# Kernel optimization log

Hardware: AMD Instinct MI355X
Metric: run time of the kernel (lower is better)

The kernel has to match this reference:

```python
import jax, jax.numpy as jnp
import numpy as np

H = 50  # hidden size

def _lstm_last_h(x, W_ih, W_hh, b_ih, b_hh):
    """Run a single-layer LSTM (PyTorch gate order i,f,g,o) over x [B,T,1],
    return final hidden state h_T [B,H]. Zero initial (h, c)."""
    B = x.shape[0]
    h0 = jnp.zeros((B, H), dtype=x.dtype)
    c0 = jnp.zeros((B, H), dtype=x.dtype)
    b = b_ih + b_hh  # [4H]

    def step(carry, xt):
        h, c = carry
        # gates: [B,4H]
        gates = xt @ W_ih.T + h @ W_hh.T + b
        i, f, g, o = jnp.split(gates, 4, axis=-1)
        i = jax.nn.sigmoid(i)
        f = jax.nn.sigmoid(f)
        g = jnp.tanh(g)
        o = jax.nn.sigmoid(o)
        c = f * c + i * g
        h = o * jnp.tanh(c)
        return (h, c), None

    xt = jnp.swapaxes(x, 0, 1)  # [T,B,1]
    (hT, _), _ = jax.lax.scan(step, (h0, c0), xt)
    return hT


def setup_inputs() -> dict:
    key = jax.random.key(0)
    ks = jax.random.split(key, 7)
    B, T = 1024, 96
    s = 1.0 / np.sqrt(H)  # PyTorch LSTM init scale
    return {
        "x": jax.random.normal(ks[0], (B, T, 1), dtype=jnp.float32),
        "W_ih": jax.random.uniform(ks[1], (4 * H, 1), jnp.float32, -s, s),
        "W_hh": jax.random.uniform(ks[2], (4 * H, H), jnp.float32, -s, s),
        "b_ih": jax.random.uniform(ks[3], (4 * H,), jnp.float32, -s, s),
        "b_hh": jax.random.uniform(ks[4], (4 * H,), jnp.float32, -s, s),
        "W_fc": jax.random.uniform(ks[5], (1, H), jnp.float32, -s, s),
        "b_fc": jax.random.uniform(ks[6], (1,), jnp.float32, -s, s),
        "num_pred": 12,
    }


def reference(x, W_ih, W_hh, b_ih, b_hh, W_fc, b_fc, num_pred):
    preds = []
    for _ in range(num_pred):  # static loop over prediction horizon
        hT = _lstm_last_h(x, W_ih, W_hh, b_ih, b_hh)        # [B,H]
        out = hT @ W_fc.T + b_fc                            # [B,1]
        preds.append(out[:, 0])
        # append prediction as next input, drop oldest timestep (window slides)
        x = jnp.concatenate([x, out[:, :, None]], axis=1)[:, 1:, :]
    return jnp.stack(preds, axis=1)  # [B, num_pred]
```

## Files before the change

### kernel.cpp

```cpp
#include <hip/hip_runtime.h>
#include <stdint.h>


#define HSZ 50
#define TLEN 96

#define GRP(WT,A0,A1,A2,A3,IL,IH,FL,FH,GL,GH,OL,OH,BL,BH,POST) \
    "s_waitcnt lgkmcnt(" WT ")\n\t" \
    "v_pk_fma_f32 v[" A0 "], v[" IL "], v[" BL "], v[" A0 "]\n\t" \
    "v_pk_fma_f32 v[" A1 "], v[" FL "], v[" BL "], v[" A1 "]\n\t" \
    "v_pk_fma_f32 v[" A2 "], v[" GL "], v[" BL "], v[" A2 "]\n\t" \
    "v_pk_fma_f32 v[" A3 "], v[" OL "], v[" BL "], v[" A3 "]\n\t" \
    "v_pk_fma_f32 v[" A0 "], v[" IH "], v[" BH "], v[" A0 "]\n\t" \
    "v_pk_fma_f32 v[" A1 "], v[" FH "], v[" BH "], v[" A1 "]\n\t" \
    "v_pk_fma_f32 v[" A2 "], v[" GH "], v[" BH "], v[" A2 "]\n\t" \
    "v_pk_fma_f32 v[" A3 "], v[" OH "], v[" BH "], v[" A3 "]\n\t" \
    POST

#define GRPM(WT,A0,A1,A2,A3,IL,IH,FL,FH,GL,GH,OL,OH,BL,BH,POST) \
    "s_waitcnt lgkmcnt(" WT ")\n\t" \
    "v_pk_mul_f32 v[" A0 "], v[" IL "], v[" BL "]\n\t" \
    "v_pk_mul_f32 v[" A1 "], v[" FL "], v[" BL "]\n\t" \
    "v_pk_mul_f32 v[" A2 "], v[" GL "], v[" BL "]\n\t" \
    "v_pk_mul_f32 v[" A3 "], v[" OL "], v[" BL "]\n\t" \
    "v_pk_fma_f32 v[" A0 "], v[" IH "], v[" BH "], v[" A0 "]\n\t" \
    "v_pk_fma_f32 v[" A1 "], v[" FH "], v[" BH "], v[" A1 "]\n\t" \
    "v_pk_fma_f32 v[" A2 "], v[" GH "], v[" BH "], v[" A2 "]\n\t" \
    "v_pk_fma_f32 v[" A3 "], v[" OH "], v[" BH "], v[" A3 "]\n\t" \
    POST

#define GRPX(...)  GRP(__VA_ARGS__)
#define GRPMX(...) GRPM(__VA_ARGS__)
#define SOLOX(...) SOLO(__VA_ARGS__)

#define PA "22:23","24:25","26:27","28:29"
#define PB "30:31","32:33","34:35","36:37"
#define PC "38:39","40:41","42:43","44:45"
#define W0  "48:49","50:51","100:101","102:103","152:153","154:155","204:205","206:207"
#define W1  "52:53","54:55","104:105","106:107","156:157","158:159","208:209","210:211"
#define W2  "56:57","58:59","108:109","110:111","160:161","162:163","212:213","214:215"
#define W3  "60:61","62:63","112:113","114:115","164:165","166:167","216:217","218:219"
#define W4  "64:65","66:67","116:117","118:119","168:169","170:171","220:221","222:223"
#define W5  "68:69","70:71","120:121","122:123","172:173","174:175","224:225","226:227"
#define W6  "72:73","74:75","124:125","126:127","176:177","178:179","228:229","230:231"
#define W7  "76:77","78:79","128:129","130:131","180:181","182:183","232:233","234:235"
#define W8  "80:81","82:83","132:133","134:135","184:185","186:187","236:237","238:239"
#define W9  "84:85","86:87","136:137","138:139","188:189","190:191","240:241","242:243"
#define W10 "88:89","90:91","140:141","142:143","192:193","194:195","244:245","246:247"
#define W11 "92:93","94:95","144:145","146:147","196:197","198:199","248:249","250:251"
#define W12 "96:97","98:99","148:149","150:151","200:201","202:203","252:253","254:255"
#define B0 "0:1","2:3"
#define B1 "4:5","6:7"
#define B2 "8:9","10:11"
#define B3 "12:13","14:15"

#define SOLO(XOFF,XW,CR,HNW,H0,H1,H2,H3,H4,H5,H6,H7,H8,H9,H10,H11,H12) \
    "ds_read_b32 v12, v19 offset:" XOFF "\n\t" \
    "s_waitcnt lgkmcnt(0)\n\t" \
    "ds_write_b32 v20, v12 offset:" XW "\n\t" \
    "ds_read_b128 v[0:3], v20 offset:" H0 "\n\t" \
    "ds_read_b128 v[4:7], v20 offset:" H1 "\n\t" \
    GRPMX("1", PA, W0, B0, "ds_read_b128 v[0:3], v20 offset:" H2 "\n\t") \
    GRPX("1", PA, W1,  B1, "ds_read_b128 v[4:7], v20 offset:" H3 "\n\t") \
    GRPX("1", PA, W2,  B0, "ds_read_b128 v[0:3], v20 offset:" H4 "\n\t") \
    GRPX("1", PA, W3,  B1, "ds_read_b128 v[4:7], v20 offset:" H5 "\n\t") \
    GRPX("1", PA, W4,  B0, "ds_read_b128 v[0:3], v20 offset:" H6 "\n\t") \
    GRPX("1", PA, W5,  B1, "ds_read_b128 v[4:7], v20 offset:" H7 "\n\t") \
    GRPX("1", PA, W6,  B0, "ds_read_b128 v[0:3], v20 offset:" H8 "\n\t") \
    GRPX("1", PA, W7,  B1, "ds_read_b128 v[4:7], v20 offset:" H9 "\n\t") \
    GRPX("1", PA, W8,  B0, "ds_read_b128 v[0:3], v20 offset:" H10 "\n\t") \
    GRPX("1", PA, W9,  B1, "ds_read_b128 v[4:7], v20 offset:" H11 "\n\t") \
    GRPX("1", PA, W10, B0, "ds_read_b128 v[0:3], v20 offset:" H12 "\n\t") \
    GRPX("1", PA, W11, B1, "") \
    GRPX("0", PA, W12, B0, "") \
    "v_add_f32 v22, v22, v23\n\t" \
    "v_add_f32 v24, v24, v25\n\t" \
    "v_add_f32 v26, v26, v27\n\t" \
    "v_add_f32 v28, v28, v29\n\t" \
    "v_mul_f32 v23, 0xbfb8aa3b, v22\n\t" \
    "v_mul_f32 v25, 0xbfb8aa3b, v24\n\t" \
    "v_mul_f32 v27, 0x4038aa3b, v26\n\t" \
    "v_mul_f32 v29, 0xbfb8aa3b, v28\n\t" \
    "v_exp_f32 v23, v23\n\t" "v_exp_f32 v25, v25\n\t" \
    "v_exp_f32 v27, v27\n\t" "v_exp_f32 v29, v29\n\t" \
    "v_add_f32 v23, 1.0, v23\n\t" "v_add_f32 v25, 1.0, v25\n\t" \
    "v_add_f32 v27, 1.0, v27\n\t" "v_add_f32 v29, 1.0, v29\n\t" \
    "v_rcp_f32 v23, v23\n\t" "v_rcp_f32 v25, v25\n\t" \
    "v_rcp_f32 v27, v27\n\t" "v_rcp_f32 v29, v29\n\t" \
    "s_nop 1\n\t" \
    "v_fma_f32 v27, -2.0, v27, 1.0\n\t" \
    "v_mul_f32 v22, v23, v27\n\t" \
    "v_fma_f32 " CR ", v25, " CR ", v22\n\t" \
    "v_mul_f32 v24, 0x4038aa3b, " CR "\n\t" \
    "v_exp_f32 v24, v24\n\t" \
    "s_nop 1\n\t" \
    "v_add_f32 v24, 1.0, v24\n\t" \
    "v_rcp_f32 v24, v24\n\t" \
    "s_nop 1\n\t" \
    "v_fma_f32 v24, -2.0, v24, 1.0\n\t" \
    "v_mul_f32 v22, v29, v24\n\t" \
    "ds_write_b32 v21, v22 offset:" HNW "\n\t"

#define HA "0","16","32","48","64","80","96","112","128","144","160","176","192"
#define HB "256","272","288","304","320","336","352","368","384","400","416","432","448"
#define HC "512","528","544","560","576","592","608","624","640","656","672","688","704"

#define FC(PREDOFF) \
    "v_mul_f32 v26, v22, v46\n\t" \
    "s_nop 1\n\t" \
    "ds_swizzle_b32 v27, v26 offset:0x041F\n\t" \
    "s_waitcnt lgkmcnt(0)\n\t" \
    "v_add_f32 v26, v26, v27\n\t" \
    "ds_swizzle_b32 v27, v26 offset:0x081F\n\t" \
    "s_waitcnt lgkmcnt(0)\n\t" \
    "v_add_f32 v26, v26, v27\n\t" \
    "ds_swizzle_b32 v27, v26 offset:0x101F\n\t" \
    "s_waitcnt lgkmcnt(0)\n\t" \
    "v_add_f32 v26, v26, v27\n\t" \
    "ds_swizzle_b32 v27, v26 offset:0x201F\n\t" \
    "s_waitcnt lgkmcnt(0)\n\t" \
    "v_add_f32 v26, v26, v27\n\t" \
    "ds_swizzle_b32 v27, v26 offset:0x401F\n\t" \
    "s_waitcnt lgkmcnt(0)\n\t" \
    "v_add_f32 v26, v26, v27\n\t" \
    "s_nop 1\n\t" \
    "v_readlane_b32 s26, v26, 0\n\t" \
    "v_readlane_b32 s27, v26, 32\n\t" \
    "s_nop 4\n\t" \
    "v_mov_b32 v27, s26\n\t" \
    "v_add_f32 v27, s27, v27\n\t" \
    "v_add_f32 v27, s25, v27\n\t" \
    "ds_write_b32 v19, v27 offset:" PREDOFF "\n\t"

__global__ __attribute__((amdgpu_flat_work_group_size(64, 64),
                          amdgpu_waves_per_eu(1, 1)))
void rec_lstm_kernel(const float* __restrict__ x,
                     const float* __restrict__ W_ih,
                     const float* __restrict__ W_hh,
                     const float* __restrict__ b_ih,
                     const float* __restrict__ b_hh,
                     const float* __restrict__ W_fc,
                     const float* __restrict__ b_fc,
                     const int*   __restrict__ num_pred,
                     float*       __restrict__ out)
{
    const int b = blockIdx.x;
    const int j = threadIdx.x;

    __shared__ __align__(16) float lds[304];
    if (j < 48) { lds[192 + j] = x[b*TLEN + j]; lds[192 + j + 48] = x[b*TLEN + j + 48]; }

    const int NP = num_pred[0];
    const int nt = NP / 3;
    const uint32_t lb = (uint32_t)(uintptr_t)&lds[0];

    asm volatile(
        "s_load_dword s25, %[bfcp], 0x0\n\t"
        "s_waitcnt lgkmcnt(0)\n\t"
        "v_mbcnt_lo_u32_b32 v0, -1, 0\n\t"
        "v_mbcnt_hi_u32_b32 v0, -1, v0\n\t"
        "s_mov_b32 s22, 49\n\t"
        "v_min_u32 v1, s22, v0\n\t"
        "s_mov_b32 s22, 200\n\t"
        "v_mul_lo_u32 v2, s22, v1\n\t"
        "s_mov_b32 s22, 10000\n\t"
        "v_add_u32 v3, s22, v2\n\t"
        "s_mov_b32 s22, 20000\n\t"
        "v_add_u32 v4, s22, v2\n\t"
        "s_mov_b32 s22, 30000\n\t"
        "v_add_u32 v5, s22, v2\n\t"
        "v_lshlrev_b32 v6, 2, v1\n\t"
        "global_load_dword v48,  v6, %[bih]\n\t"
        "global_load_dword v100, v6, %[bih] offset:200\n\t"
        "global_load_dword v152, v6, %[bih] offset:400\n\t"
        "global_load_dword v204, v6, %[bih] offset:600\n\t"
        "global_load_dword v7,  v6, %[bhh]\n\t"
        "global_load_dword v8,  v6, %[bhh] offset:200\n\t"
        "global_load_dword v9,  v6, %[bhh] offset:400\n\t"
        "global_load_dword v10, v6, %[bhh] offset:600\n\t"
        "global_load_dword v49,  v6, %[wih]\n\t"
        "global_load_dword v101, v6, %[wih] offset:200\n\t"
        "global_load_dword v153, v6, %[wih] offset:400\n\t"
        "global_load_dword v205, v6, %[wih] offset:600\n\t"
        "global_load_dword v46, v6, %[wfcp]\n\t"
        "global_load_dwordx4 v[50:53], v2, %[whh]\n\t"
        "global_load_dwordx4 v[54:57], v2, %[whh] offset:16\n\t"
        "global_load_dwordx4 v[58:61], v2, %[whh] offset:32\n\t"
        "global_load_dwordx4 v[62:65], v2, %[whh] offset:48\n\t"
        "global_load_dwordx4 v[66:69], v2, %[whh] offset:64\n\t"
        "global_load_dwordx4 v[70:73], v2, %[whh] offset:80\n\t"
        "global_load_dwordx4 v[74:77], v2, %[whh] offset:96\n\t"
        "global_load_dwordx4 v[78:81], v2, %[whh] offset:112\n\t"
        "global_load_dwordx4 v[82:85], v2, %[whh] offset:128\n\t"
        "global_load_dwordx4 v[86:89], v2, %[whh] offset:144\n\t"
        "global_load_dwordx4 v[90:93], v2, %[whh] offset:160\n\t"
        "global_load_dwordx4 v[94:97], v2, %[whh] offset:176\n\t"
        "global_load_dwordx2 v[98:99], v2, %[whh] offset:192\n\t"
        "global_load_dwordx4 v[102:105], v3, %[whh]\n\t"
        "global_load_dwordx4 v[106:109], v3, %[whh] offset:16\n\t"
        "global_load_dwordx4 v[110:113], v3, %[whh] offset:32\n\t"
        "global_load_dwordx4 v[114:117], v3, %[whh] offset:48\n\t"
        "global_load_dwordx4 v[118:121], v3, %[whh] offset:64\n\t"
        "global_load_dwordx4 v[122:125], v3, %[whh] offset:80\n\t"
        "global_load_dwordx4 v[126:129], v3, %[whh] offset:96\n\t"
        "global_load_dwordx4 v[130:133], v3, %[whh] offset:112\n\t"
        "global_load_dwordx4 v[134:137], v3, %[whh] offset:128\n\t"
        "global_load_dwordx4 v[138:141], v3, %[whh] offset:144\n\t"
        "global_load_dwordx4 v[142:145], v3, %[whh] offset:160\n\t"
        "global_load_dwordx4 v[146:149], v3, %[whh] offset:176\n\t"
        "global_load_dwordx2 v[150:151], v3, %[whh] offset:192\n\t"
        "global_load_dwordx4 v[154:157], v4, %[whh]\n\t"
        "global_load_dwordx4 v[158:161], v4, %[whh] offset:16\n\t"
        "global_load_dwordx4 v[162:165], v4, %[whh] offset:32\n\t"
        "global_load_dwordx4 v[166:169], v4, %[whh] offset:48\n\t"
        "global_load_dwordx4 v[170:173], v4, %[whh] offset:64\n\t"
        "global_load_dwordx4 v[174:177], v4, %[whh] offset:80\n\t"
        "global_load_dwordx4 v[178:181], v4, %[whh] offset:96\n\t"
        "global_load_dwordx4 v[182:185], v4, %[whh] offset:112\n\t"
        "global_load_dwordx4 v[186:189], v4, %[whh] offset:128\n\t"
        "global_load_dwordx4 v[190:193], v4, %[whh] offset:144\n\t"
        "global_load_dwordx4 v[194:197], v4, %[whh] offset:160\n\t"
        "global_load_dwordx4 v[198:201], v4, %[whh] offset:176\n\t"
        "global_load_dwordx2 v[202:203], v4, %[whh] offset:192\n\t"
        "global_load_dwordx4 v[206:209], v5, %[whh]\n\t"
        "global_load_dwordx4 v[210:213], v5, %[whh] offset:16\n\t"
        "global_load_dwordx4 v[214:217], v5, %[whh] offset:32\n\t"
        "global_load_dwordx4 v[218:221], v5, %[whh] offset:48\n\t"
        "global_load_dwordx4 v[222:225], v5, %[whh] offset:64\n\t"
        "global_load_dwordx4 v[226:229], v5, %[whh] offset:80\n\t"
        "global_load_dwordx4 v[230:233], v5, %[whh] offset:96\n\t"
        "global_load_dwordx4 v[234:237], v5, %[whh] offset:112\n\t"
        "global_load_dwordx4 v[238:241], v5, %[whh] offset:128\n\t"
        "global_load_dwordx4 v[242:245], v5, %[whh] offset:144\n\t"
        "global_load_dwordx4 v[246:249], v5, %[whh] offset:160\n\t"
        "global_load_dwordx4 v[250:253], v5, %[whh] offset:176\n\t"
        "global_load_dwordx2 v[254:255], v5, %[whh] offset:192\n\t"
        "s_waitcnt vmcnt(0)\n\t"
        "v_add_f32 v48,  v48,  v7\n\t"
        "v_add_f32 v100, v100, v8\n\t"
        "v_add_f32 v152, v152, v9\n\t"
        "v_add_f32 v204, v204, v10\n\t"
        "v_cmp_gt_u32 vcc, 50, v0\n\t"
        "v_cndmask_b32 v46, 0, v46, vcc\n\t"
        "v_mov_b32 v20, %[lb]\n\t"
        "v_lshl_add_u32 v21, v1, 2, v20\n\t"
        "v_add_u32 v21, 8, v21\n\t"
        "v_add_u32 v19, 0x300, v20\n\t"
        "s_mov_b32 s21, %[nt]\n\t"
        "4:\n\t"
        "v_mov_b32 v16, 0\n\t"
        "v_mov_b32 v17, 0\n\t"
        "v_mov_b32 v18, 0\n\t"
        "v_mov_b32 v5, 0\n\t"
        "v_mov_b32 v6, 1.0\n\t"
        "ds_write_b32 v21, v5\n\t"
        "ds_write_b32 v21, v5 offset:256\n\t"
        "ds_write_b32 v21, v5 offset:512\n\t"
        "ds_write_b32 v20, v6\n\t"
        "ds_write_b32 v20, v6 offset:256\n\t"
        "ds_write_b32 v20, v6 offset:512\n\t"
        "ds_read_b32 v12, v19 offset:0\n\t"
        "ds_read_b32 v13, v19 offset:4\n\t"
        "ds_read_b32 v14, v19 offset:8\n\t"
        "s_waitcnt lgkmcnt(0)\n\t"
        "ds_write_b32 v20, v12 offset:4\n\t"
        "ds_write_b32 v20, v13 offset:260\n\t"
        "ds_write_b32 v20, v14 offset:516\n\t"
        "v_add_u32 v19, 4, v19\n\t"
        "ds_read_b128 v[0:3],   v20 offset:0\n\t"
        "ds_read_b128 v[4:7],   v20 offset:256\n\t"
        "ds_read_b128 v[8:11],  v20 offset:512\n\t"
        "ds_read_b128 v[12:15], v20 offset:16\n\t"
        "s_mov_b32 s20, 94\n\t"
        "3:\n\t"
        GRPMX("3", PA, W0,  B0, "ds_read_b128 v[0:3],   v20 offset:272\n\t")
        GRPMX("3", PB, W0,  B1, "ds_read_b128 v[4:7],   v20 offset:528\n\t")
        GRPMX("3", PC, W0,  B2, "ds_read_b128 v[8:11],  v20 offset:32\n\t")
        GRPX("3", PA, W1,  B3, "ds_read_b128 v[12:15], v20 offset:288\n\t")
        GRPX("3", PB, W1,  B0, "ds_read_b128 v[0:3],   v20 offset:544\n\t")
        GRPX("3", PC, W1,  B1, "ds_read_b128 v[4:7],   v20 offset:48\n\t")
        GRPX("3", PA, W2,  B2, "ds_read_b128 v[8:11],  v20 offset:304\n\t")
        GRPX("3", PB, W2,  B3, "ds_read_b128 v[12:15], v20 offset:560\n\t")
        GRPX("3", PC, W2,  B0, "ds_read_b128 v[0:3],   v20 offset:64\n\t")
        GRPX("3", PA, W3,  B1, "ds_read_b128 v[4:7],   v20 offset:320\n\t")
        GRPX("3", PB, W3,  B2, "ds_read_b128 v[8:11],  v20 offset:576\n\t")
        GRPX("3", PC, W3,  B3, "ds_read_b128 v[12:15], v20 offset:80\n\t")
        GRPX("3", PA, W4,  B0, "ds_read_b128 v[0:3],   v20 offset:336\n\t")
        GRPX("3", PB, W4,  B1, "ds_read_b128 v[4:7],   v20 offset:592\n\t")
        GRPX("3", PC, W4,  B2, "ds_read_b128 v[8:11],  v20 offset:96\n\t")
        GRPX("3", PA, W5,  B3, "ds_read_b128 v[12:15], v20 offset:352\n\t")
        GRPX("3", PB, W5,  B0, "ds_read_b128 v[0:3],   v20 offset:608\n\t")
        GRPX("3", PC, W5,  B1, "ds_read_b128 v[4:7],   v20 offset:112\n\t")
        GRPX("3", PA, W6,  B2, "ds_read_b128 v[8:11],  v20 offset:368\n\t")
        GRPX("3", PB, W6,  B3, "ds_read_b128 v[12:15], v20 offset:624\n\t")
        GRPX("3", PC, W6,  B0, "ds_read_b128 v[0:3],   v20 offset:128\n\t")
        GRPX("3", PA, W7,  B1, "ds_read_b128 v[4:7],   v20 offset:384\n\t")
        GRPX("3", PB, W7,  B2, "ds_read_b128 v[8:11],  v20 offset:640\n\t")
        GRPX("3", PC, W7,  B3, "ds_read_b128 v[12:15], v20 offset:144\n\t")
        GRPX("3", PA, W8,  B0, "ds_read_b128 v[0:3],   v20 offset:400\n\t")
        GRPX("3", PB, W8,  B1, "ds_read_b128 v[4:7],   v20 offset:656\n\t")
        GRPX("3", PC, W8,  B2, "ds_read_b128 v[8:11],  v20 offset:160\n\t")
        GRPX("3", PA, W9,  B3, "ds_read_b128 v[12:15], v20 offset:416\n\t")
        GRPX("3", PB, W9,  B0, "ds_read_b128 v[0:3],   v20 offset:672\n\t")
        GRPX("3", PC, W9,  B1, "ds_read_b128 v[4:7],   v20 offset:176\n\t")
        GRPX("3", PA, W10, B2, "ds_read_b128 v[8:11],  v20 offset:432\n\t")
        GRPX("3", PB, W10, B3, "ds_read_b128 v[12:15], v20 offset:688\n\t")
        GRPX("3", PC, W10, B0, "ds_read_b128 v[0:3],   v20 offset:192\n\t")
        GRPX("3", PA, W11, B1, "ds_read_b128 v[4:7],   v20 offset:448\n\t")
        GRPX("3", PB, W11, B2, "ds_read_b128 v[8:11],  v20 offset:704\n\t")
        GRPX("3", PC, W11, B3, "")
        "ds_read_b32 v12, v19 offset:0\n\t"
        "ds_read_b32 v13, v19 offset:4\n\t"
        "ds_read_b32 v14, v19 offset:8\n\t"
        GRPX("5", PA, W12, B0, "")
        GRPX("4", PB, W12, B1, "")
        GRPX("3", PC, W12, B2, "")
        "v_add_f32 v22, v22, v23\n\t" "v_add_f32 v24, v24, v25\n\t"
        "v_add_f32 v26, v26, v27\n\t" "v_add_f32 v28, v28, v29\n\t"
        "v_add_f32 v30, v30, v31\n\t" "v_add_f32 v32, v32, v33\n\t"
        "v_add_f32 v34, v34, v35\n\t" "v_add_f32 v36, v36, v37\n\t"
        "v_add_f32 v38, v38, v39\n\t" "v_add_f32 v40, v40, v41\n\t"
        "v_add_f32 v42, v42, v43\n\t" "v_add_f32 v44, v44, v45\n\t"
        "v_mul_f32 v23, 0xbfb8aa3b, v22\n\t"
        "v_mul_f32 v31, 0xbfb8aa3b, v30\n\t"
        "v_mul_f32 v39, 0xbfb8aa3b, v38\n\t"
        "v_mul_f32 v25, 0xbfb8aa3b, v24\n\t"
        "v_mul_f32 v33, 0xbfb8aa3b, v32\n\t"
        "v_mul_f32 v41, 0xbfb8aa3b, v40\n\t"
        "v_mul_f32 v27, 0x4038aa3b, v26\n\t"
        "v_mul_f32 v35, 0x4038aa3b, v34\n\t"
        "v_mul_f32 v43, 0x4038aa3b, v42\n\t"
        "v_mul_f32 v29, 0xbfb8aa3b, v28\n\t"
        "v_mul_f32 v37, 0xbfb8aa3b, v36\n\t"
        "v_mul_f32 v45, 0xbfb8aa3b, v44\n\t"
        "v_exp_f32 v23, v23\n\t" "v_exp_f32 v31, v31\n\t" "v_exp_f32 v39, v39\n\t"
        "v_exp_f32 v25, v25\n\t" "v_exp_f32 v33, v33\n\t" "v_exp_f32 v41, v41\n\t"
        "v_exp_f32 v27, v27\n\t" "v_exp_f32 v35, v35\n\t" "v_exp_f32 v43, v43\n\t"
        "v_exp_f32 v29, v29\n\t" "v_exp_f32 v37, v37\n\t" "v_exp_f32 v45, v45\n\t"
        "v_add_f32 v23, 1.0, v23\n\t" "v_add_f32 v31, 1.0, v31\n\t" "v_add_f32 v39, 1.0, v39\n\t"
        "v_add_f32 v25, 1.0, v25\n\t" "v_add_f32 v33, 1.0, v33\n\t" "v_add_f32 v41, 1.0, v41\n\t"
        "v_add_f32 v27, 1.0, v27\n\t" "v_add_f32 v35, 1.0, v35\n\t" "v_add_f32 v43, 1.0, v43\n\t"
        "v_add_f32 v29, 1.0, v29\n\t" "v_add_f32 v37, 1.0, v37\n\t" "v_add_f32 v45, 1.0, v45\n\t"
        "v_rcp_f32 v23, v23\n\t" "v_rcp_f32 v31, v31\n\t" "v_rcp_f32 v39, v39\n\t"
        "v_rcp_f32 v25, v25\n\t" "v_rcp_f32 v33, v33\n\t" "v_rcp_f32 v41, v41\n\t"
        "v_rcp_f32 v27, v27\n\t" "v_rcp_f32 v35, v35\n\t" "v_rcp_f32 v43, v43\n\t"
        "v_rcp_f32 v29, v29\n\t" "v_rcp_f32 v37, v37\n\t" "v_rcp_f32 v45, v45\n\t"
        "v_fma_f32 v27, -2.0, v27, 1.0\n\t"
        "v_fma_f32 v35, -2.0, v35, 1.0\n\t"
        "v_fma_f32 v43, -2.0, v43, 1.0\n\t"
        "v_mul_f32 v22, v23, v27\n\t"
        "v_mul_f32 v30, v31, v35\n\t"
        "v_mul_f32 v38, v39, v43\n\t"
        "v_fma_f32 v16, v25, v16, v22\n\t"
        "v_fma_f32 v17, v33, v17, v30\n\t"
        "v_fma_f32 v18, v41, v18, v38\n\t"
        "v_mul_f32 v24, 0x4038aa3b, v16\n\t"
        "v_mul_f32 v32, 0x4038aa3b, v17\n\t"
        "v_mul_f32 v40, 0x4038aa3b, v18\n\t"
        "v_exp_f32 v24, v24\n\t" "v_exp_f32 v32, v32\n\t" "v_exp_f32 v40, v40\n\t"
        "v_add_f32 v24, 1.0, v24\n\t" "v_add_f32 v32, 1.0, v32\n\t" "v_add_f32 v40, 1.0, v40\n\t"
        "v_rcp_f32 v24, v24\n\t" "v_rcp_f32 v32, v32\n\t" "v_rcp_f32 v40, v40\n\t"
        "s_nop 0\n\t"
        "v_fma_f32 v24, -2.0, v24, 1.0\n\t"
        "v_fma_f32 v32, -2.0, v32, 1.0\n\t"
        "v_fma_f32 v40, -2.0, v40, 1.0\n\t"
        "v_mul_f32 v22, v29, v24\n\t"
        "v_mul_f32 v30, v37, v32\n\t"
        "v_mul_f32 v38, v45, v40\n\t"
        "ds_write_b32 v21, v22\n\t"
        "ds_write_b32 v21, v30 offset:256\n\t"
        "ds_write_b32 v21, v38 offset:512\n\t"
        "s_waitcnt lgkmcnt(3)\n\t"
        "ds_write_b32 v20, v12 offset:4\n\t"
        "ds_write_b32 v20, v13 offset:260\n\t"
        "ds_write_b32 v20, v14 offset:516\n\t"
        "v_add_u32 v19, 4, v19\n\t"
        "ds_read_b128 v[0:3],   v20 offset:0\n\t"
        "ds_read_b128 v[4:7],   v20 offset:256\n\t"
        "ds_read_b128 v[8:11],  v20 offset:512\n\t"
        "ds_read_b128 v[12:15], v20 offset:16\n\t"
        "s_sub_u32 s20, s20, 1\n\t"
        "s_cmp_lg_u32 s20, 0\n\t"
        "s_cbranch_scc1 3b\n\t"
        "s_waitcnt lgkmcnt(0)\n\t"
        "v_add_u32 v19, -8, v19\n\t"
        SOLOX("4",  "4",   "v16", "0",   HA)
        SOLOX("8",  "4",   "v16", "0",   HA)
        FC("12")
        SOLOX("8",  "260", "v17", "256", HB)
        SOLOX("12", "260", "v17", "256", HB)
        FC("16")
        SOLOX("12", "516", "v18", "512", HC)
        SOLOX("16", "516", "v18", "512", HC)
        FC("20")
        "s_waitcnt lgkmcnt(0)\n\t"
        "v_add_u32 v19, 0xfffffe98, v19\n\t"
        "s_sub_u32 s21, s21, 1\n\t"
        "s_cmp_lg_u32 s21, 0\n\t"
        "s_cbranch_scc1 4b\n\t"
        :
        : [lb] "v"(lb), [nt] "s"(nt),
          [whh] "s"(W_hh), [wih] "s"(W_ih), [bih] "s"(b_ih), [bhh] "s"(b_hh),
          [wfcp] "s"(W_fc), [bfcp] "s"(b_fc)
        : "memory", "scc", "vcc", "s20", "s21", "s22", "s25", "s26", "s27",
          "v0","v1","v2","v3","v4","v5","v6","v7","v8","v9","v10","v11",
          "v12","v13","v14","v15","v16","v17","v18","v19","v20","v21","v22",
          "v23","v24","v25","v26","v27","v28","v29","v30","v31","v32","v33",
          "v34","v35","v36","v37","v38","v39","v40","v41","v42","v43","v44",
          "v45","v46",
          "v48","v49","v50","v51","v52","v53","v54","v55","v56","v57","v58",
          "v59","v60","v61","v62","v63","v64","v65","v66","v67","v68","v69",
          "v70","v71","v72","v73","v74","v75","v76","v77","v78","v79","v80",
          "v81","v82","v83","v84","v85","v86","v87","v88","v89","v90","v91",
          "v92","v93","v94","v95","v96","v97","v98","v99","v100","v101",
          "v102","v103","v104","v105","v106","v107","v108","v109","v110",
          "v111","v112","v113","v114","v115","v116","v117","v118","v119",
          "v120","v121","v122","v123","v124","v125","v126","v127","v128",
          "v129","v130","v131","v132","v133","v134","v135","v136","v137",
          "v138","v139","v140","v141","v142","v143","v144","v145","v146",
          "v147","v148","v149","v150","v151","v152","v153","v154","v155",
          "v156","v157","v158","v159","v160","v161","v162","v163","v164",
          "v165","v166","v167","v168","v169","v170","v171","v172","v173",
          "v174","v175","v176","v177","v178","v179","v180","v181","v182",
          "v183","v184","v185","v186","v187","v188","v189","v190","v191",
          "v192","v193","v194","v195","v196","v197","v198","v199","v200",
          "v201","v202","v203","v204","v205","v206","v207","v208","v209",
          "v210","v211","v212","v213","v214","v215","v216","v217","v218",
          "v219","v220","v221","v222","v223","v224","v225","v226","v227",
          "v228","v229","v230","v231","v232","v233","v234","v235","v236",
          "v237","v238","v239","v240","v241","v242","v243","v244","v245",
          "v246","v247","v248","v249","v250","v251","v252","v253","v254",
          "v255");

    if (j < NP) out[b * NP + j] = lds[192 + TLEN + j];
}

extern "C" void kernel_launch(void* const* d_in, const int* in_sizes, int n_in,
                              void* d_out, int out_size, void* d_ws, size_t ws_size,
                              hipStream_t stream)
{
    const float* x    = (const float*)d_in[0];
    const float* W_ih = (const float*)d_in[1];
    const float* W_hh = (const float*)d_in[2];
    const float* b_ih = (const float*)d_in[3];
    const float* b_hh = (const float*)d_in[4];
    const float* W_fc = (const float*)d_in[5];
    const float* b_fc = (const float*)d_in[6];
    const int*   np   = (const int*)d_in[7];
    float* out = (float*)d_out;

    const int B = in_sizes[0] / TLEN;
    rec_lstm_kernel<<<B, 64, 0, stream>>>(x, W_ih, W_hh, b_ih, b_hh,
                                          W_fc, b_fc, np, out);
}
```

Baseline: 495.1 us.

## Replace three-chain interleaved LSTM recurrence with single chain and deeper LDS prefetch

The old kernel interleaved three independent prediction chains (PA/PB/PC) so one chain's math could hide another's latency, then ran serial SOLO steps at the tail. The new code runs one prediction at a time with a single accumulator set. It issues all seven h-vector LDS reads up front, with more in flight per step, and drops the staggered SOLO tail logic. This gives a simpler schedule and fewer LDS buffers, but removes the instruction-level parallelism that hid the latency of the exp/rcp and LDS round-trip on the serial dependence chain.

```diff
diff --git a/kernel.cpp b/kernel.cpp
--- a/kernel.cpp
+++ b/kernel.cpp
@@ -16,7 +16,6 @@
     "v_pk_fma_f32 v[" A2 "], v[" GH "], v[" BH "], v[" A2 "]\n\t" \
     "v_pk_fma_f32 v[" A3 "], v[" OH "], v[" BH "], v[" A3 "]\n\t" \
     POST
-
 #define GRPM(WT,A0,A1,A2,A3,IL,IH,FL,FH,GL,GH,OL,OH,BL,BH,POST) \
     "s_waitcnt lgkmcnt(" WT ")\n\t" \
     "v_pk_mul_f32 v[" A0 "], v[" IL "], v[" BL "]\n\t" \
@@ -28,14 +27,10 @@
     "v_pk_fma_f32 v[" A2 "], v[" GH "], v[" BH "], v[" A2 "]\n\t" \
     "v_pk_fma_f32 v[" A3 "], v[" OH "], v[" BH "], v[" A3 "]\n\t" \
     POST
-
 #define GRPX(...)  GRP(__VA_ARGS__)
 #define GRPMX(...) GRPM(__VA_ARGS__)
-#define SOLOX(...) SOLO(__VA_ARGS__)
-
-#define PA "22:23","24:25","26:27","28:29"
-#define PB "30:31","32:33","34:35","36:37"
-#define PC "38:39","40:41","42:43","44:45"
+
+#define ACC "28:29","30:31","32:33","34:35"
 #define W0  "48:49","50:51","100:101","102:103","152:153","154:155","204:205","206:207"
 #define W1  "52:53","54:55","104:105","106:107","156:157","158:159","208:209","210:211"
 #define W2  "56:57","58:59","108:109","110:111","160:161","162:163","212:213","214:215"
@@ -49,88 +44,13 @@
 #define W10 "88:89","90:91","140:141","142:143","192:193","194:195","244:245","246:247"
 #define W11 "92:93","94:95","144:145","146:147","196:197","198:199","248:249","250:251"
 #define W12 "96:97","98:99","148:149","150:151","200:201","202:203","252:253","254:255"
-#define B0 "0:1","2:3"
-#define B1 "4:5","6:7"
-#define B2 "8:9","10:11"
-#define B3 "12:13","14:15"
-
-#define SOLO(XOFF,XW,CR,HNW,H0,H1,H2,H3,H4,H5,H6,H7,H8,H9,H10,H11,H12) \
-    "ds_read_b32 v12, v19 offset:" XOFF "\n\t" \
-    "s_waitcnt lgkmcnt(0)\n\t" \
-    "ds_write_b32 v20, v12 offset:" XW "\n\t" \
-    "ds_read_b128 v[0:3], v20 offset:" H0 "\n\t" \
-    "ds_read_b128 v[4:7], v20 offset:" H1 "\n\t" \
-    GRPMX("1", PA, W0, B0, "ds_read_b128 v[0:3], v20 offset:" H2 "\n\t") \
-    GRPX("1", PA, W1,  B1, "ds_read_b128 v[4:7], v20 offset:" H3 "\n\t") \
-    GRPX("1", PA, W2,  B0, "ds_read_b128 v[0:3], v20 offset:" H4 "\n\t") \
-    GRPX("1", PA, W3,  B1, "ds_read_b128 v[4:7], v20 offset:" H5 "\n\t") \
-    GRPX("1", PA, W4,  B0, "ds_read_b128 v[0:3], v20 offset:" H6 "\n\t") \
-    GRPX("1", PA, W5,  B1, "ds_read_b128 v[4:7], v20 offset:" H7 "\n\t") \
-    GRPX("1", PA, W6,  B0, "ds_read_b128 v[0:3], v20 offset:" H8 "\n\t") \
-    GRPX("1", PA, W7,  B1, "ds_read_b128 v[4:7], v20 offset:" H9 "\n\t") \
-    GRPX("1", PA, W8,  B0, "ds_read_b128 v[0:3], v20 offset:" H10 "\n\t") \
-    GRPX("1", PA, W9,  B1, "ds_read_b128 v[4:7], v20 offset:" H11 "\n\t") \
-    GRPX("1", PA, W10, B0, "ds_read_b128 v[0:3], v20 offset:" H12 "\n\t") \
-    GRPX("1", PA, W11, B1, "") \
-    GRPX("0", PA, W12, B0, "") \
-    "v_add_f32 v22, v22, v23\n\t" \
-    "v_add_f32 v24, v24, v25\n\t" \
-    "v_add_f32 v26, v26, v27\n\t" \
-    "v_add_f32 v28, v28, v29\n\t" \
-    "v_mul_f32 v23, 0xbfb8aa3b, v22\n\t" \
-    "v_mul_f32 v25, 0xbfb8aa3b, v24\n\t" \
-    "v_mul_f32 v27, 0x4038aa3b, v26\n\t" \
-    "v_mul_f32 v29, 0xbfb8aa3b, v28\n\t" \
-    "v_exp_f32 v23, v23\n\t" "v_exp_f32 v25, v25\n\t" \
-    "v_exp_f32 v27, v27\n\t" "v_exp_f32 v29, v29\n\t" \
-    "v_add_f32 v23, 1.0, v23\n\t" "v_add_f32 v25, 1.0, v25\n\t" \
-    "v_add_f32 v27, 1.0, v27\n\t" "v_add_f32 v29, 1.0, v29\n\t" \
-    "v_rcp_f32 v23, v23\n\t" "v_rcp_f32 v25, v25\n\t" \
-    "v_rcp_f32 v27, v27\n\t" "v_rcp_f32 v29, v29\n\t" \
-    "s_nop 1\n\t" \
-    "v_fma_f32 v27, -2.0, v27, 1.0\n\t" \
-    "v_mul_f32 v22, v23, v27\n\t" \
-    "v_fma_f32 " CR ", v25, " CR ", v22\n\t" \
-    "v_mul_f32 v24, 0x4038aa3b, " CR "\n\t" \
-    "v_exp_f32 v24, v24\n\t" \
-    "s_nop 1\n\t" \
-    "v_add_f32 v24, 1.0, v24\n\t" \
-    "v_rcp_f32 v24, v24\n\t" \
-    "s_nop 1\n\t" \
-    "v_fma_f32 v24, -2.0, v24, 1.0\n\t" \
-    "v_mul_f32 v22, v29, v24\n\t" \
-    "ds_write_b32 v21, v22 offset:" HNW "\n\t"
-
-#define HA "0","16","32","48","64","80","96","112","128","144","160","176","192"
-#define HB "256","272","288","304","320","336","352","368","384","400","416","432","448"
-#define HC "512","528","544","560","576","592","608","624","640","656","672","688","704"
-
-#define FC(PREDOFF) \
-    "v_mul_f32 v26, v22, v46\n\t" \
-    "s_nop 1\n\t" \
-    "ds_swizzle_b32 v27, v26 offset:0x041F\n\t" \
-    "s_waitcnt lgkmcnt(0)\n\t" \
-    "v_add_f32 v26, v26, v27\n\t" \
-    "ds_swizzle_b32 v27, v26 offset:0x081F\n\t" \
-    "s_waitcnt lgkmcnt(0)\n\t" \
-    "v_add_f32 v26, v26, v27\n\t" \
-    "ds_swizzle_b32 v27, v26 offset:0x101F\n\t" \
-    "s_waitcnt lgkmcnt(0)\n\t" \
-    "v_add_f32 v26, v26, v27\n\t" \
-    "ds_swizzle_b32 v27, v26 offset:0x201F\n\t" \
-    "s_waitcnt lgkmcnt(0)\n\t" \
-    "v_add_f32 v26, v26, v27\n\t" \
-    "ds_swizzle_b32 v27, v26 offset:0x401F\n\t" \
-    "s_waitcnt lgkmcnt(0)\n\t" \
-    "v_add_f32 v26, v26, v27\n\t" \
-    "s_nop 1\n\t" \
-    "v_readlane_b32 s26, v26, 0\n\t" \
-    "v_readlane_b32 s27, v26, 32\n\t" \
-    "s_nop 4\n\t" \
-    "v_mov_b32 v27, s26\n\t" \
-    "v_add_f32 v27, s27, v27\n\t" \
-    "v_add_f32 v27, s25, v27\n\t" \
-    "ds_write_b32 v19, v27 offset:" PREDOFF "\n\t"
+#define SL0 "0:1","2:3"
+#define SL1 "4:5","6:7"
+#define SL2 "8:9","10:11"
+#define SL3 "12:13","14:15"
+#define SL4 "16:17","18:19"
+#define SL5 "20:21","22:23"
+#define SL6 "24:25","26:27"
 
 __global__ __attribute__((amdgpu_flat_work_group_size(64, 64),
                           amdgpu_waves_per_eu(1, 1)))
@@ -147,11 +67,10 @@
     const int b = blockIdx.x;
     const int j = threadIdx.x;
 
-    __shared__ __align__(16) float lds[304];
-    if (j < 48) { lds[192 + j] = x[b*TLEN + j]; lds[192 + j + 48] = x[b*TLEN + j + 48]; }
+    __shared__ __align__(16) float lds[176];
+    if (j < 48) { lds[64 + j] = x[b*TLEN + j]; lds[64 + j + 48] = x[b*TLEN + j + 48]; }
 
     const int NP = num_pred[0];
-    const int nt = NP / 3;
     const uint32_t lb = (uint32_t)(uintptr_t)&lds[0];
 
     asm volatile(
@@ -182,7 +101,7 @@
         "global_load_dword v101, v6, %[wih] offset:200\n\t"
         "global_load_dword v153, v6, %[wih] offset:400\n\t"
         "global_load_dword v205, v6, %[wih] offset:600\n\t"
-        "global_load_dword v46, v6, %[wfcp]\n\t"
+        "global_load_dword v41, v6, %[wfcp]\n\t"
         "global_load_dwordx4 v[50:53], v2, %[whh]\n\t"
         "global_load_dwordx4 v[54:57], v2, %[whh] offset:16\n\t"
         "global_load_dwordx4 v[58:61], v2, %[whh] offset:32\n\t"
@@ -241,165 +160,121 @@
         "v_add_f32 v152, v152, v9\n\t"
         "v_add_f32 v204, v204, v10\n\t"
         "v_cmp_gt_u32 vcc, 50, v0\n\t"
-        "v_cndmask_b32 v46, 0, v46, vcc\n\t"
-        "v_mov_b32 v20, %[lb]\n\t"
-        "v_lshl_add_u32 v21, v1, 2, v20\n\t"
-        "v_add_u32 v21, 8, v21\n\t"
-        "v_add_u32 v19, 0x300, v20\n\t"
-        "s_mov_b32 s21, %[nt]\n\t"
+        "v_cndmask_b32 v41, 0, v41, vcc\n\t"
+        "v_mov_b32 v38, %[lb]\n\t"
+        "v_lshl_add_u32 v39, v1, 2, v38\n\t"
+        "v_add_u32 v39, 8, v39\n\t"
+        "v_add_u32 v40, 0x100, v38\n\t"
+        "v_mov_b32 v44, 1.0\n\t"
+        "ds_write_b32 v38, v44\n\t"
+        "s_mov_b32 s21, %[np]\n\t"
         "4:\n\t"
-        "v_mov_b32 v16, 0\n\t"
-        "v_mov_b32 v17, 0\n\t"
-        "v_mov_b32 v18, 0\n\t"
-        "v_mov_b32 v5, 0\n\t"
-        "v_mov_b32 v6, 1.0\n\t"
-        "ds_write_b32 v21, v5\n\t"
-        "ds_write_b32 v21, v5 offset:256\n\t"
-        "ds_write_b32 v21, v5 offset:512\n\t"
-        "ds_write_b32 v20, v6\n\t"
-        "ds_write_b32 v20, v6 offset:256\n\t"
-        "ds_write_b32 v20, v6 offset:512\n\t"
-        "ds_read_b32 v12, v19 offset:0\n\t"
-        "ds_read_b32 v13, v19 offset:4\n\t"
-        "ds_read_b32 v14, v19 offset:8\n\t"
-        "s_waitcnt lgkmcnt(0)\n\t"
-        "ds_write_b32 v20, v12 offset:4\n\t"
-        "ds_write_b32 v20, v13 offset:260\n\t"
-        "ds_write_b32 v20, v14 offset:516\n\t"
-        "v_add_u32 v19, 4, v19\n\t"
-        "ds_read_b128 v[0:3],   v20 offset:0\n\t"
-        "ds_read_b128 v[4:7],   v20 offset:256\n\t"
-        "ds_read_b128 v[8:11],  v20 offset:512\n\t"
-        "ds_read_b128 v[12:15], v20 offset:16\n\t"
-        "s_mov_b32 s20, 94\n\t"
+        "v_mov_b32 v36, 0\n\t"
+        "v_mov_b32 v44, 0\n\t"
+        "ds_write_b32 v39, v44\n\t"
+        "ds_read_b32 v42, v40\n\t"
+        "s_waitcnt lgkmcnt(0)\n\t"
+        "ds_write_b32 v38, v42 offset:4\n\t"
+        "ds_read_b128 v[0:3],   v38 offset:0\n\t"
+        "ds_read_b128 v[4:7],   v38 offset:16\n\t"
+        "ds_read_b128 v[8:11],  v38 offset:32\n\t"
+        "ds_read_b128 v[12:15], v38 offset:48\n\t"
+        "ds_read_b128 v[16:19], v38 offset:64\n\t"
+        "ds_read_b128 v[20:23], v38 offset:80\n\t"
+        "ds_read_b128 v[24:27], v38 offset:96\n\t"
+        "s_mov_b32 s20, 96\n\t"
         "3:\n\t"
-        GRPMX("3", PA, W0,  B0, "ds_read_b128 v[0:3],   v20 offset:272\n\t")
-        GRPMX("3", PB, W0,  B1, "ds_read_b128 v[4:7],   v20 offset:528\n\t")
-        GRPMX("3", PC, W0,  B2, "ds_read_b128 v[8:11],  v20 offset:32\n\t")
-        GRPX("3", PA, W1,  B3, "ds_read_b128 v[12:15], v20 offset:288\n\t")
-        GRPX("3", PB, W1,  B0, "ds_read_b128 v[0:3],   v20 offset:544\n\t")
-        GRPX("3", PC, W1,  B1, "ds_read_b128 v[4:7],   v20 offset:48\n\t")
-        GRPX("3", PA, W2,  B2, "ds_read_b128 v[8:11],  v20 offset:304\n\t")
-        GRPX("3", PB, W2,  B3, "ds_read_b128 v[12:15], v20 offset:560\n\t")
-        GRPX("3", PC, W2,  B0, "ds_read_b128 v[0:3],   v20 offset:64\n\t")
-        GRPX("3", PA, W3,  B1, "ds_read_b128 v[4:7],   v20 offset:320\n\t")
-        GRPX("3", PB, W3,  B2, "ds_read_b128 v[8:11],  v20 offset:576\n\t")
-        GRPX("3", PC, W3,  B3, "ds_read_b128 v[12:15], v20 offset:80\n\t")
-        GRPX("3", PA, W4,  B0, "ds_read_b128 v[0:3],   v20 offset:336\n\t")
-        GRPX("3", PB, W4,  B1, "ds_read_b128 v[4:7],   v20 offset:592\n\t")
-        GRPX("3", PC, W4,  B2, "ds_read_b128 v[8:11],  v20 offset:96\n\t")
-        GRPX("3", PA, W5,  B3, "ds_read_b128 v[12:15], v20 offset:352\n\t")
-        GRPX("3", PB, W5,  B0, "ds_read_b128 v[0:3],   v20 offset:608\n\t")
-        GRPX("3", PC, W5,  B1, "ds_read_b128 v[4:7],   v20 offset:112\n\t")
-        GRPX("3", PA, W6,  B2, "ds_read_b128 v[8:11],  v20 offset:368\n\t")
-        GRPX("3", PB, W6,  B3, "ds_read_b128 v[12:15], v20 offset:624\n\t")
-        GRPX("3", PC, W6,  B0, "ds_read_b128 v[0:3],   v20 offset:128\n\t")
-        GRPX("3", PA, W7,  B1, "ds_read_b128 v[4:7],   v20 offset:384\n\t")
-        GRPX("3", PB, W7,  B2, "ds_read_b128 v[8:11],  v20 offset:640\n\t")
-        GRPX("3", PC, W7,  B3, "ds_read_b128 v[12:15], v20 offset:144\n\t")
-        GRPX("3", PA, W8,  B0, "ds_read_b128 v[0:3],   v20 offset:400\n\t")
-        GRPX("3", PB, W8,  B1, "ds_read_b128 v[4:7],   v20 offset:656\n\t")
-        GRPX("3", PC, W8,  B2, "ds_read_b128 v[8:11],  v20 offset:160\n\t")
-        GRPX("3", PA, W9,  B3, "ds_read_b128 v[12:15], v20 offset:416\n\t")
-        GRPX("3", PB, W9,  B0, "ds_read_b128 v[0:3],   v20 offset:672\n\t")
-        GRPX("3", PC, W9,  B1, "ds_read_b128 v[4:7],   v20 offset:176\n\t")
-        GRPX("3", PA, W10, B2, "ds_read_b128 v[8:11],  v20 offset:432\n\t")
-        GRPX("3", PB, W10, B3, "ds_read_b128 v[12:15], v20 offset:688\n\t")
-        GRPX("3", PC, W10, B0, "ds_read_b128 v[0:3],   v20 offset:192\n\t")
-        GRPX("3", PA, W11, B1, "ds_read_b128 v[4:7],   v20 offset:448\n\t")
-        GRPX("3", PB, W11, B2, "ds_read_b128 v[8:11],  v20 offset:704\n\t")
-        GRPX("3", PC, W11, B3, "")
-        "ds_read_b32 v12, v19 offset:0\n\t"
-        "ds_read_b32 v13, v19 offset:4\n\t"
-        "ds_read_b32 v14, v19 offset:8\n\t"
-        GRPX("5", PA, W12, B0, "")
-        GRPX("4", PB, W12, B1, "")
-        GRPX("3", PC, W12, B2, "")
-        "v_add_f32 v22, v22, v23\n\t" "v_add_f32 v24, v24, v25\n\t"
-        "v_add_f32 v26, v26, v27\n\t" "v_add_f32 v28, v28, v29\n\t"
-        "v_add_f32 v30, v30, v31\n\t" "v_add_f32 v32, v32, v33\n\t"
-        "v_add_f32 v34, v34, v35\n\t" "v_add_f32 v36, v36, v37\n\t"
-        "v_add_f32 v38, v38, v39\n\t" "v_add_f32 v40, v40, v41\n\t"
-        "v_add_f32 v42, v42, v43\n\t" "v_add_f32 v44, v44, v45\n\t"
-        "v_mul_f32 v23, 0xbfb8aa3b, v22\n\t"
+        "ds_read_b32 v42, v40 offset:4\n\t"
+        GRPMX("7", ACC, W0,  SL0, "ds_read_b128 v[0:3],   v38 offset:112\n\t")
+        GRPX("7",  ACC, W1,  SL1, "ds_read_b128 v[4:7],   v38 offset:128\n\t")
+        GRPX("7",  ACC, W2,  SL2, "ds_read_b128 v[8:11],  v38 offset:144\n\t")
+        GRPX("7",  ACC, W3,  SL3, "ds_read_b128 v[12:15], v38 offset:160\n\t")
+        GRPX("7",  ACC, W4,  SL4, "ds_read_b128 v[16:19], v38 offset:176\n\t")
+        GRPX("7",  ACC, W5,  SL5, "ds_read_b128 v[20:23], v38 offset:192\n\t")
+        GRPX("7",  ACC, W6,  SL6, "")
+        GRPX("5",  ACC, W7,  SL0, "")
+        GRPX("4",  ACC, W8,  SL1, "")
+        GRPX("3",  ACC, W9,  SL2, "")
+        GRPX("2",  ACC, W10, SL3, "")
+        GRPX("1",  ACC, W11, SL4, "")
+        GRPX("0",  ACC, W12, SL5, "")
+        "v_add_f32 v28, v28, v29\n\t"
+        "v_add_f32 v30, v30, v31\n\t"
+        "v_add_f32 v32, v32, v33\n\t"
+        "v_add_f32 v34, v34, v35\n\t"
+        "v_mul_f32 v29, 0xbfb8aa3b, v28\n\t"
         "v_mul_f32 v31, 0xbfb8aa3b, v30\n\t"
-        "v_mul_f32 v39, 0xbfb8aa3b, v38\n\t"
-        "v_mul_f32 v25, 0xbfb8aa3b, v24\n\t"
-        "v_mul_f32 v33, 0xbfb8aa3b, v32\n\t"
-        "v_mul_f32 v41, 0xbfb8aa3b, v40\n\t"
-        "v_mul_f32 v27, 0x4038aa3b, v26\n\t"
-        "v_mul_f32 v35, 0x4038aa3b, v34\n\t"
-        "v_mul_f32 v43, 0x4038aa3b, v42\n\t"
-        "v_mul_f32 v29, 0xbfb8aa3b, v28\n\t"
-        "v_mul_f32 v37, 0xbfb8aa3b, v36\n\t"
-        "v_mul_f32 v45, 0xbfb8aa3b, v44\n\t"
-        "v_exp_f32 v23, v23\n\t" "v_exp_f32 v31, v31\n\t" "v_exp_f32 v39, v39\n\t"
-        "v_exp_f32 v25, v25\n\t" "v_exp_f32 v33, v33\n\t" "v_exp_f32 v41, v41\n\t"
-        "v_exp_f32 v27, v27\n\t" "v_exp_f32 v35, v35\n\t" "v_exp_f32 v43, v43\n\t"
-        "v_exp_f32 v29, v29\n\t" "v_exp_f32 v37, v37\n\t" "v_exp_f32 v45, v45\n\t"
-        "v_add_f32 v23, 1.0, v23\n\t" "v_add_f32 v31, 1.0, v31\n\t" "v_add_f32 v39, 1.0, v39\n\t"
-        "v_add_f32 v25, 1.0, v25\n\t" "v_add_f32 v33, 1.0, v33\n\t" "v_add_f32 v41, 1.0, v41\n\t"
-        "v_add_f32 v27, 1.0, v27\n\t" "v_add_f32 v35, 1.0, v35\n\t" "v_add_f32 v43, 1.0, v43\n\t"
-        "v_add_f32 v29, 1.0, v29\n\t" "v_add_f32 v37, 1.0, v37\n\t" "v_add_f32 v45, 1.0, v45\n\t"
-        "v_rcp_f32 v23, v23\n\t" "v_rcp_f32 v31, v31\n\t" "v_rcp_f32 v39, v39\n\t"
-        "v_rcp_f32 v25, v25\n\t" "v_rcp_f32 v33, v33\n\t" "v_rcp_f32 v41, v41\n\t"
-        "v_rcp_f32 v27, v27\n\t" "v_rcp_f32 v35, v35\n\t" "v_rcp_f32 v43, v43\n\t"
-        "v_rcp_f32 v29, v29\n\t" "v_rcp_f32 v37, v37\n\t" "v_rcp_f32 v45, v45\n\t"
-        "v_fma_f32 v27, -2.0, v27, 1.0\n\t"
-        "v_fma_f32 v35, -2.0, v35, 1.0\n\t"
-        "v_fma_f32 v43, -2.0, v43, 1.0\n\t"
-        "v_mul_f32 v22, v23, v27\n\t"
-        "v_mul_f32 v30, v31, v35\n\t"
-        "v_mul_f32 v38, v39, v43\n\t"
-        "v_fma_f32 v16, v25, v16, v22\n\t"
-        "v_fma_f32 v17, v33, v17, v30\n\t"
-        "v_fma_f32 v18, v41, v18, v38\n\t"
-        "v_mul_f32 v24, 0x4038aa3b, v16\n\t"
-        "v_mul_f32 v32, 0x4038aa3b, v17\n\t"
-        "v_mul_f32 v40, 0x4038aa3b, v18\n\t"
-        "v_exp_f32 v24, v24\n\t" "v_exp_f32 v32, v32\n\t" "v_exp_f32 v40, v40\n\t"
-        "v_add_f32 v24, 1.0, v24\n\t" "v_add_f32 v32, 1.0, v32\n\t" "v_add_f32 v40, 1.0, v40\n\t"
-        "v_rcp_f32 v24, v24\n\t" "v_rcp_f32 v32, v32\n\t" "v_rcp_f32 v40, v40\n\t"
-        "s_nop 0\n\t"
-        "v_fma_f32 v24, -2.0, v24, 1.0\n\t"
-        "v_fma_f32 v32, -2.0, v32, 1.0\n\t"
-        "v_fma_f32 v40, -2.0, v40, 1.0\n\t"
-        "v_mul_f32 v22, v29, v24\n\t"
-        "v_mul_f32 v30, v37, v32\n\t"
-        "v_mul_f32 v38, v45, v40\n\t"
-        "ds_write_b32 v21, v22\n\t"
-        "ds_write_b32 v21, v30 offset:256\n\t"
-        "ds_write_b32 v21, v38 offset:512\n\t"
-        "s_waitcnt lgkmcnt(3)\n\t"
-        "ds_write_b32 v20, v12 offset:4\n\t"
-        "ds_write_b32 v20, v13 offset:260\n\t"
-        "ds_write_b32 v20, v14 offset:516\n\t"
-        "v_add_u32 v19, 4, v19\n\t"
-        "ds_read_b128 v[0:3],   v20 offset:0\n\t"
-        "ds_read_b128 v[4:7],   v20 offset:256\n\t"
-        "ds_read_b128 v[8:11],  v20 offset:512\n\t"
-        "ds_read_b128 v[12:15], v20 offset:16\n\t"
+        "v_mul_f32 v33, 0x4038aa3b, v32\n\t"
+        "v_mul_f32 v35, 0xbfb8aa3b, v34\n\t"
+        "v_exp_f32 v29, v29\n\t"
+        "v_exp_f32 v31, v31\n\t"
+        "v_exp_f32 v33, v33\n\t"
+        "v_exp_f32 v35, v35\n\t"
+        "v_add_f32 v29, 1.0, v29\n\t"
+        "v_add_f32 v31, 1.0, v31\n\t"
+        "v_add_f32 v33, 1.0, v33\n\t"
+        "v_add_f32 v35, 1.0, v35\n\t"
+        "v_rcp_f32 v29, v29\n\t"
+        "v_rcp_f32 v31, v31\n\t"
+        "v_rcp_f32 v33, v33\n\t"
+        "v_rcp_f32 v35, v35\n\t"
+        "s_nop 1\n\t"
+        "v_fma_f32 v33, -2.0, v33, 1.0\n\t"
+        "v_mul_f32 v29, v29, v33\n\t"
+        "v_fma_f32 v36, v31, v36, v29\n\t"
+        "v_mul_f32 v31, 0x4038aa3b, v36\n\t"
+        "v_exp_f32 v31, v31\n\t"
+        "s_nop 1\n\t"
+        "v_add_f32 v31, 1.0, v31\n\t"
+        "v_rcp_f32 v31, v31\n\t"
+        "s_nop 1\n\t"
+        "v_fma_f32 v31, -2.0, v31, 1.0\n\t"
+        "v_mul_f32 v37, v35, v31\n\t"
+        "ds_write_b32 v39, v37\n\t"
+        "ds_write_b32 v38, v42 offset:4\n\t"
+        "ds_read_b128 v[0:3],   v38 offset:0\n\t"
+        "ds_read_b128 v[4:7],   v38 offset:16\n\t"
+        "ds_read_b128 v[8:11],  v38 offset:32\n\t"
+        "ds_read_b128 v[12:15], v38 offset:48\n\t"
+        "ds_read_b128 v[16:19], v38 offset:64\n\t"
+        "ds_read_b128 v[20:23], v38 offset:80\n\t"
+        "ds_read_b128 v[24:27], v38 offset:96\n\t"
+        "v_add_u32 v40, 4, v40\n\t"
         "s_sub_u32 s20, s20, 1\n\t"
         "s_cmp_lg_u32 s20, 0\n\t"
         "s_cbranch_scc1 3b\n\t"
-        "s_waitcnt lgkmcnt(0)\n\t"
-        "v_add_u32 v19, -8, v19\n\t"
-        SOLOX("4",  "4",   "v16", "0",   HA)
-        SOLOX("8",  "4",   "v16", "0",   HA)
-        FC("12")
-        SOLOX("8",  "260", "v17", "256", HB)
-        SOLOX("12", "260", "v17", "256", HB)
-        FC("16")
-        SOLOX("12", "516", "v18", "512", HC)
-        SOLOX("16", "516", "v18", "512", HC)
-        FC("20")
-        "s_waitcnt lgkmcnt(0)\n\t"
-        "v_add_u32 v19, 0xfffffe98, v19\n\t"
+        "v_mul_f32 v44, v37, v41\n\t"
+        "s_nop 1\n\t"
+        "ds_swizzle_b32 v45, v44 offset:0x041F\n\t"
+        "s_waitcnt lgkmcnt(0)\n\t"
+        "v_add_f32 v44, v44, v45\n\t"
+        "ds_swizzle_b32 v45, v44 offset:0x081F\n\t"
+        "s_waitcnt lgkmcnt(0)\n\t"
+        "v_add_f32 v44, v44, v45\n\t"
+        "ds_swizzle_b32 v45, v44 offset:0x101F\n\t"
+        "s_waitcnt lgkmcnt(0)\n\t"
+        "v_add_f32 v44, v44, v45\n\t"
+        "ds_swizzle_b32 v45, v44 offset:0x201F\n\t"
+        "s_waitcnt lgkmcnt(0)\n\t"
+        "v_add_f32 v44, v44, v45\n\t"
+        "ds_swizzle_b32 v45, v44 offset:0x401F\n\t"
+        "s_waitcnt lgkmcnt(0)\n\t"
+        "v_add_f32 v44, v44, v45\n\t"
+        "s_nop 1\n\t"
+        "v_readlane_b32 s26, v44, 0\n\t"
+        "v_readlane_b32 s27, v44, 32\n\t"
+        "s_nop 4\n\t"
+        "v_mov_b32 v45, s26\n\t"
+        "v_add_f32 v45, s27, v45\n\t"
+        "v_add_f32 v45, s25, v45\n\t"
+        "ds_write_b32 v40, v45\n\t"
+        "s_waitcnt lgkmcnt(0)\n\t"
+        "v_add_u32 v40, 0xfffffe84, v40\n\t"
         "s_sub_u32 s21, s21, 1\n\t"
         "s_cmp_lg_u32 s21, 0\n\t"
         "s_cbranch_scc1 4b\n\t"
         :
-        : [lb] "v"(lb), [nt] "s"(nt),
+        : [lb] "v"(lb), [np] "s"(NP),
           [whh] "s"(W_hh), [wih] "s"(W_ih), [bih] "s"(b_ih), [bhh] "s"(b_hh),
           [wfcp] "s"(W_fc), [bfcp] "s"(b_fc)
         : "memory", "scc", "vcc", "s20", "s21", "s22", "s25", "s26", "s27",
@@ -407,7 +282,7 @@
           "v12","v13","v14","v15","v16","v17","v18","v19","v20","v21","v22",
           "v23","v24","v25","v26","v27","v28","v29","v30","v31","v32","v33",
           "v34","v35","v36","v37","v38","v39","v40","v41","v42","v43","v44",
-          "v45","v46",
+          "v45",
           "v48","v49","v50","v51","v52","v53","v54","v55","v56","v57","v58",
           "v59","v60","v61","v62","v63","v64","v65","v66","v67","v68","v69",
           "v70","v71","v72","v73","v74","v75","v76","v77","v78","v79","v80",
@@ -432,7 +307,7 @@
           "v246","v247","v248","v249","v250","v251","v252","v253","v254",
           "v255");
 
-    if (j < NP) out[b * NP + j] = lds[192 + TLEN + j];
+    if (j < NP) out[b * NP + j] = lds[64 + TLEN + j];
 }
 
 extern "C" void kernel_launch(void* const* d_in, const int* in_sizes, int n_in,
```

Measured after the change: 501.4 us. About the same (+1.3%).
